# Kernel tuning notes

Measured on AMD Instinct MI355X. Metric: run time of the kernel, lower is better.

The kernel has to match this reference:

```python
import jax, jax.numpy as jnp
import numpy as np

VOCAB, D_MODEL, HEADS, PAD_ID = 32000, 512, 8, 0
D_K = D_MODEL // HEADS
EPS = 1e-5


def pos_encoding(T, d):
    pos = jnp.arange(T, dtype=jnp.float32)[:, None]              # [T,1]
    freqs = 1.0 / (10000.0 ** (jnp.arange(0, d, 2, dtype=jnp.float32) / d))
    ang = pos * freqs                                            # [T,d/2]
    pe = jnp.zeros((T, d), dtype=jnp.float32)
    pe = pe.at[:, 0::2].set(jnp.sin(ang)).at[:, 1::2].set(jnp.cos(ang))
    return pe


def layer_norm(x, g, b):
    mu = jnp.mean(x, axis=-1, keepdims=True)
    var = jnp.var(x, axis=-1, keepdims=True)
    return (x - mu) * jax.lax.rsqrt(var + EPS) * g + b


def setup_inputs() -> dict:
    key = jax.random.key(0)
    ks = jax.random.split(key, 12)
    B, T = 4, 2048
    s = 0.02
    inp = {
        "tokens": jax.random.randint(ks[0], (B, T), 0, VOCAB),
        "emb": jax.random.normal(ks[1], (VOCAB, D_MODEL), jnp.float32) * s,
        "wq": jax.random.normal(ks[2], (D_MODEL, D_MODEL), jnp.float32) * s,
        "bq": jnp.zeros((D_MODEL,), jnp.float32),
        "wk": jax.random.normal(ks[3], (D_MODEL, D_MODEL), jnp.float32) * s,
        "bk": jnp.zeros((D_MODEL,), jnp.float32),
        "wv": jax.random.normal(ks[4], (D_MODEL, D_MODEL), jnp.float32) * s,
        "bv": jnp.zeros((D_MODEL,), jnp.float32),
        "wo": jax.random.normal(ks[5], (D_MODEL, D_MODEL), jnp.float32) * s,
        "bo": jnp.zeros((D_MODEL,), jnp.float32),
        "w1": jax.random.normal(ks[6], (D_MODEL, 2 * D_MODEL), jnp.float32) * s,
        "b1": jnp.zeros((2 * D_MODEL,), jnp.float32),
        "w2": jax.random.normal(ks[7], (2 * D_MODEL, D_MODEL), jnp.float32) * s,
        "b2": jnp.zeros((D_MODEL,), jnp.float32),
        "ln1_g": jnp.ones((D_MODEL,), jnp.float32),
        "ln1_b": jnp.zeros((D_MODEL,), jnp.float32),
        "ln2_g": jnp.ones((D_MODEL,), jnp.float32),
        "ln2_b": jnp.zeros((D_MODEL,), jnp.float32),
    }
    return inp


def reference(tokens, emb, wq, bq, wk, bk, wv, bv, wo, bo,
              w1, b1, w2, b2, ln1_g, ln1_b, ln2_g, ln2_b):
    B, T = tokens.shape
    x = emb[tokens] * jnp.sqrt(jnp.float32(D_MODEL))             # [B,T,D]
    x = x + pos_encoding(T, D_MODEL)[None]                       # add PE
    q = (x @ wq + bq).reshape(B, T, HEADS, D_K)
    k = (x @ wk + bk).reshape(B, T, HEADS, D_K)
    v = (x @ wv + bv).reshape(B, T, HEADS, D_K)
    scores = jnp.einsum("bqhd,bkhd->bhqk", q, k) / jnp.sqrt(jnp.float32(D_K))
    key_pad_mask = tokens == PAD_ID                              # [B,T]
    neg = jnp.finfo(scores.dtype).min
    scores = jnp.where(key_pad_mask[:, None, None, :], neg, scores)
    attn = jax.nn.softmax(scores, axis=-1)                       # [B,H,T,T]
    av = jnp.einsum("bhqk,bkhd->bqhd", attn, v).reshape(B, T, D_MODEL)
    av = av @ wo + bo
    h = layer_norm(av + x, ln1_g, ln1_b)
    ff = jax.nn.relu(h @ w1 + b1) @ w2 + b2
    out = layer_norm(h + ff, ln2_g, ln2_b)
    return out, key_pad_mask
```

## Files before the change

kernel.cpp:

```cpp
#include <hip/hip_runtime.h>
#include <hip/hip_bf16.h>
#include <math.h>

#define D_MODEL 512
#define HEADS   8
#define D_K     64
#define T_SEQ   2048
#define B_SZ    4
#define NROWS   (B_SZ * T_SEQ)
#define KVB     64
#define KSPLIT  2
#define KHALF   (T_SEQ / KSPLIT)

#define BKG 64

typedef __attribute__((ext_vector_type(8))) short short8;
typedef __attribute__((ext_vector_type(4))) float f32x4;
typedef __attribute__((ext_vector_type(4))) ushort bf16x4;
typedef __attribute__((ext_vector_type(4))) unsigned int u32x4;

typedef __attribute__((address_space(1))) const unsigned int as1_uint;
typedef __attribute__((address_space(3))) unsigned int as3_uint;

__device__ __forceinline__ ushort f2bf(float f) {
    union { float f; unsigned u; } v; v.f = f;
    unsigned u = v.u;
    unsigned r = (u + 0x7FFFu + ((u >> 16) & 1u)) >> 16;
    return (ushort)r;
}
__device__ __forceinline__ float bf2f(ushort u) {
    union { unsigned u; float f; } v; v.u = ((unsigned)u) << 16;
    return v.f;
}
__device__ __forceinline__ unsigned pk_bf16(float lo, float hi) {
    unsigned r;
    asm("v_cvt_pk_bf16_f32 %0, %1, %2" : "=v"(r) : "v"(lo), "v"(hi));
    return r;
}

__global__ __launch_bounds__(256) void k_prep(
    const int* __restrict__ tokens, const float* __restrict__ emb,
    const float* __restrict__ wq, const float* __restrict__ wk,
    const float* __restrict__ wv, const float* __restrict__ wo,
    const float* __restrict__ w1, const float* __restrict__ w2,
    const float* __restrict__ bq, const float* __restrict__ bk,
    const float* __restrict__ bv,
    ushort* __restrict__ xb, float* __restrict__ mask_out,
    ushort* __restrict__ wqkvT, ushort* __restrict__ woT,
    ushort* __restrict__ w1T, ushort* __restrict__ w2T,
    float* __restrict__ bqkv, float qsc)
{
    __shared__ ushort tls[32][33];
    int bid = blockIdx.x, tid = threadIdx.x;
    if (bid < 4096) {
        int row = bid * 2 + (tid >> 7);
        int t   = row & (T_SEQ - 1);
        int tok = tokens[row];
        int t2  = tid & 127;
        if (t2 == 0) mask_out[row] = (tok == 0) ? 1.0f : 0.0f;
        const float* e = emb + (size_t)tok * D_MODEL;
#pragma unroll
        for (int i = 0; i < 4; ++i) {
            int d = t2 + 128 * i;
            float freq = exp2f(-(float)(d & ~1) * 0.025952563240330564f);
            float sn, cs;
            __sincosf((float)t * freq, &sn, &cs);
            float x = e[d] * 22.627416997969522f + ((d & 1) ? cs : sn);
            xb[(size_t)row * D_MODEL + d] = f2bf(x);
        }
        return;
    }
    const float* src; ushort* dst; float scale = 1.0f; int K, N, bx, by;
    if (bid < 5120) {
        int b = bid - 4096; int z = b >> 8; int rem = b & 255;
        bx = rem & 15; by = rem >> 4; K = 512; N = 512;
        src = (z == 0) ? wq : (z == 1) ? wk : (z == 2) ? wv : wo;
        dst = (z < 3) ? wqkvT + (size_t)z * 512 * 512 : woT;
        scale = (z == 0) ? qsc : 1.0f;
    } else if (bid < 5632) {
        int b = bid - 5120; bx = b & 31; by = b >> 5; K = 512; N = 1024; src = w1; dst = w1T;
    } else if (bid < 6144) {
        int b = bid - 5632; bx = b & 15; by = b >> 4; K = 1024; N = 512; src = w2; dst = w2T;
    } else {
        int i = (bid - 6144) * 256 + tid;
        if (i < 512)       bqkv[i] = bq[i] * qsc;
        else if (i < 1024) bqkv[i] = bk[i - 512];
        else if (i < 1536) bqkv[i] = bv[i - 1024];
        return;
    }
    int tx = tid & 31, ty = tid >> 5;
    int n0 = bx * 32, k0 = by * 32;
#pragma unroll
    for (int i = 0; i < 4; ++i)
        tls[ty + i * 8][tx] = f2bf(src[(size_t)(k0 + ty + i * 8) * N + n0 + tx] * scale);
    __syncthreads();
#pragma unroll
    for (int i = 0; i < 4; ++i)
        dst[(size_t)(n0 + ty + i * 8) * K + k0 + tx] = tls[tx][ty + i * 8];
}

template<int MODE, bool RELU, int BMT, int BNT, bool COMBA>
__global__ __launch_bounds__(256) void k_gemm_lds(
    const ushort* __restrict__ A, const ushort* __restrict__ A2,
    const float* __restrict__ lpb,
    const ushort* __restrict__ BT,
    const float* __restrict__ bias, void* __restrict__ C0,
    void* __restrict__ C1, void* __restrict__ C2,
    int M, int N, int K)
{
    constexpr int MR = BMT / 32;
    constexpr int NR = BNT / 32;
    __shared__ __attribute__((aligned(16))) ushort As[2][BMT * BKG];
    __shared__ __attribute__((aligned(16))) ushort Bs[2][BNT * BKG];

    const int tid = threadIdx.x;
    const int w = tid >> 6, l = tid & 63;
    const int lr = l & 15, lg = l >> 4;
    const int wr = w >> 1, wc = w & 1;

    int bx = blockIdx.x, by = blockIdx.y;
    {
        int nx = gridDim.x, ny = gridDim.y;
        if ((ny & 7) == 0) {
            int lin = bx + nx * by;
            int xcd = lin & 7, idx = lin >> 3;
            int per = ny >> 3;
            by = xcd * per + (idx % per);
            bx = idx / per;
        }
    }
    const int brow0 = by * BMT;
    const int bcol0 = bx * BNT;
    const int swz = lr & 7;

    f32x4 acc[MR][NR] = {};
    const int nks = K >> 6;

#define STAGE_B(buf, k0)                                                        \
    {                                                                           \
        _Pragma("unroll")                                                       \
        for (int i = 0; i < BNT / 32; ++i) {                                    \
            int gi = w * (BNT * 2) + i * 64 + l;                                \
            int row = gi >> 3, slot = gi & 7;                                   \
            int g = slot ^ (row & 7);                                           \
            __builtin_amdgcn_global_load_lds(                                   \
                (as1_uint*)(BT + (size_t)(bcol0 + row) * K + (k0) + g * 8),     \
                (as3_uint*)(&Bs[buf][gi * 8]), 16, 0, 0);                       \
        }                                                                       \
    }
#define STAGE_A_DMA(buf, k0)                                                    \
    {                                                                           \
        _Pragma("unroll")                                                       \
        for (int i = 0; i < BMT / 32; ++i) {                                    \
            int gi = w * (BMT * 2) + i * 64 + l;                                \
            int row = gi >> 3, slot = gi & 7;                                   \
            int g = slot ^ (row & 7);                                           \
            __builtin_amdgcn_global_load_lds(                                   \
                (as1_uint*)(A + (size_t)(brow0 + row) * K + (k0) + g * 8),      \
                (as3_uint*)(&As[buf][gi * 8]), 16, 0, 0);                       \
        }                                                                       \
    }
#define STAGE_A_COMB(buf, k0)                                                   \
    {                                                                           \
        int head = (k0) >> 6;                                                   \
        _Pragma("unroll")                                                       \
        for (int i = 0; i < BMT / 32; ++i) {                                    \
            int gi = w * (BMT * 2) + i * 64 + l;                                \
            int row = gi >> 3, slot = gi & 7;                                   \
            int g = slot ^ (row & 7);                                           \
            size_t off = (size_t)(brow0 + row) * K + (k0) + g * 8;              \
            bf16x4 a0 = *(const bf16x4*)(A + off);                              \
            bf16x4 a1 = *(const bf16x4*)(A + off + 4);                          \
            bf16x4 c0 = *(const bf16x4*)(A2 + off);                             \
            bf16x4 c1 = *(const bf16x4*)(A2 + off + 4);                         \
            float l0 = lpb[(size_t)head * NROWS + brow0 + row];                 \
            float l1 = lpb[(size_t)(8 + head) * NROWS + brow0 + row];           \
            float r = 1.0f / (l0 + l1);                                         \
            u32x4 pk;                                                           \
            pk[0] = pk_bf16((bf2f(a0[0]) + bf2f(c0[0])) * r,                    \
                            (bf2f(a0[1]) + bf2f(c0[1])) * r);                   \
            pk[1] = pk_bf16((bf2f(a0[2]) + bf2f(c0[2])) * r,                    \
                            (bf2f(a0[3]) + bf2f(c0[3])) * r);                   \
            pk[2] = pk_bf16((bf2f(a1[0]) + bf2f(c1[0])) * r,                    \
                            (bf2f(a1[1]) + bf2f(c1[1])) * r);                   \
            pk[3] = pk_bf16((bf2f(a1[2]) + bf2f(c1[2])) * r,                    \
                            (bf2f(a1[3]) + bf2f(c1[3])) * r);                   \
            *(u32x4*)(&As[buf][gi * 8]) = pk;                                   \
        }                                                                       \
    }
#define STAGE(buf, k0)                                                          \
    {                                                                           \
        if constexpr (COMBA) { STAGE_A_COMB(buf, k0); }                         \
        else                 { STAGE_A_DMA(buf, k0); }                          \
        STAGE_B(buf, k0);                                                       \
    }

    STAGE(0, 0);
    __syncthreads();

    int buf = 0;
    for (int ks = 0; ks < nks; ++ks) {
        if (ks + 1 < nks) STAGE(buf ^ 1, (ks + 1) * BKG);
#pragma unroll
        for (int kk = 0; kk < 2; ++kk) {
            short8 af[MR], bfr[NR];
#pragma unroll
            for (int m = 0; m < MR; ++m) {
                int row = wr * (BMT / 2) + m * 16 + lr;
                int slot = (kk * 4 + lg) ^ swz;
                af[m] = *(const short8*)(&As[buf][row * 64 + slot * 8]);
            }
#pragma unroll
            for (int n = 0; n < NR; ++n) {
                int row = wc * (BNT / 2) + n * 16 + lr;
                int slot = (kk * 4 + lg) ^ swz;
                bfr[n] = *(const short8*)(&Bs[buf][row * 64 + slot * 8]);
            }
#pragma unroll
            for (int m = 0; m < MR; ++m)
#pragma unroll
                for (int n = 0; n < NR; ++n)
                    acc[m][n] = __builtin_amdgcn_mfma_f32_16x16x32_bf16(af[m], bfr[n], acc[m][n], 0, 0, 0);
        }
        __syncthreads();
        buf ^= 1;
    }
#undef STAGE
#undef STAGE_A_COMB
#undef STAGE_A_DMA
#undef STAGE_B

#pragma unroll
    for (int n = 0; n < NR; ++n) {
        int col = bcol0 + wc * (BNT / 2) + n * 16 + lr;
        float bv = bias[col];
#pragma unroll
        for (int m = 0; m < MR; ++m) {
            int row0 = brow0 + wr * (BMT / 2) + m * 16 + 4 * lg;
            if constexpr (MODE == 2) {
                int seg = col >> 9, lc = col & 511;
                if (seg == 2) {
                    bf16x4 pk;
#pragma unroll
                    for (int j = 0; j < 4; ++j) pk[j] = f2bf(acc[m][n][j] + bv);
                    *(bf16x4*)((ushort*)C2 + (size_t)lc * M + row0) = pk;
                } else {
                    ushort* dst = (seg == 0) ? (ushort*)C0 : (ushort*)C1;
#pragma unroll
                    for (int j = 0; j < 4; ++j)
                        dst[(size_t)(row0 + j) * 512 + lc] = f2bf(acc[m][n][j] + bv);
                }
            } else if constexpr (MODE == 0) {
#pragma unroll
                for (int j = 0; j < 4; ++j) {
                    float v = acc[m][n][j] + bv;
                    if (RELU) v = fmaxf(v, 0.0f);
                    ((ushort*)C0)[(size_t)(row0 + j) * N + col] = f2bf(v);
                }
            } else {
#pragma unroll
                for (int j = 0; j < 4; ++j)
                    ((float*)C0)[(size_t)(row0 + j) * N + col] = acc[m][n][j] + bv;
            }
        }
    }
}

__global__ __launch_bounds__(512, 4) void k_attn(
    const ushort* __restrict__ Q, const ushort* __restrict__ Kb,
    const ushort* __restrict__ Vt, const int* __restrict__ tokens,
    ushort* __restrict__ O0, ushort* __restrict__ O1,
    float* __restrict__ lp)
{
    __shared__ __attribute__((aligned(16))) ushort Kl[2][KVB * 64];
    __shared__ __attribute__((aligned(16))) ushort Vl[2][KVB * 64];
    __shared__ __attribute__((aligned(16))) ushort Mbh[KHALF];
    __shared__ int padf[KHALF / KVB];

    const int tid = threadIdx.x;
    const int w = tid >> 6, l = tid & 63;
    const int lr = l & 15, lg = l >> 4;
    const int swz = lr & 7;

    int lin = blockIdx.x + 8 * (blockIdx.y + 8 * blockIdx.z);
    int xcd = lin & 7, idx = lin >> 3;
    int qt  = idx & 7;
    int grp = xcd + 8 * (idx >> 3);
    int ks  = grp & 1;
    int h   = (grp >> 1) & 7;
    int b   = grp >> 4;

    const int q0  = qt * 256 + w * 32;
    const int kb0 = ks * KHALF;

    const int gi   = w * 64 + l;
    const int srow = gi >> 3;
    const int sg   = gi & 7;
    const int sgx  = sg ^ (srow & 7);
    const ushort* Ksrc = Kb + ((size_t)(b * T_SEQ + kb0) + srow) * D_MODEL + h * D_K + sgx * 8;
    const int kbase = 32 * (sg >> 2) + 8 * ((sg >> 1) & 1) + 4 * (sg & 1);
    const ushort* Vsrc = Vt + (size_t)(h * D_K + srow) * NROWS + b * T_SEQ + kb0 + kbase;
    const int vds = srow * 128 + sgx * 16;

#define KSTAGE(bufi, kt_)                                                       \
    __builtin_amdgcn_global_load_lds(                                           \
        (as1_uint*)(Ksrc + (size_t)(kt_) * KVB * D_MODEL),                      \
        (as3_uint*)(&Kl[bufi][gi * 8]), 16, 0, 0);

    const ushort* Qh = Q + (size_t)b * T_SEQ * D_MODEL + h * D_K;
    short8 aq[2][2];
#pragma unroll
    for (int qs = 0; qs < 2; ++qs)
#pragma unroll
        for (int c2 = 0; c2 < 2; ++c2)
            aq[qs][c2] = *(const short8*)(Qh + (size_t)(q0 + qs * 16 + lr) * D_MODEL
                                          + c2 * 32 + 8 * lg);

    short8 vones;
#pragma unroll
    for (int i = 0; i < 8; ++i) vones[i] = (short)0x3F80;

    const int* tk = tokens + b * T_SEQ + kb0;
#pragma unroll
    for (int it = 0; it < KHALF / 512; ++it) {
        int i = tid + it * 512;
        bool pad = (tk[i] == 0);
        Mbh[i] = pad ? (ushort)0xFF7F : (ushort)0;
        unsigned long long bal = __ballot(pad);
        if (l == 0) padf[it * 8 + w] = (bal != 0ull);
    }

    f32x4 acc[2][4] = {};
    f32x4 acc_l[2] = {};

    {
        bf16x4 va = *(const bf16x4*)(Vsrc);
        bf16x4 vb2 = *(const bf16x4*)(Vsrc + 16);
        KSTAGE(0, 0);
        u32x4 pk = { ((const unsigned*)&va)[0], ((const unsigned*)&va)[1],
                     ((const unsigned*)&vb2)[0], ((const unsigned*)&vb2)[1] };
        *(u32x4*)((char*)Vl[0] + vds) = pk;
    }
    __syncthreads();

    int buf = 0;
    const int NT = KHALF / KVB;
#pragma unroll 2
    for (int kt = 0; kt < NT; ++kt) {
        bf16x4 vna, vnb;
        bool more = (kt + 1 < NT);
        if (more) {
            KSTAGE(buf ^ 1, kt + 1);
            vna = *(const bf16x4*)(Vsrc + (kt + 1) * KVB);
            vnb = *(const bf16x4*)(Vsrc + (kt + 1) * KVB + 16);
        }

        const ushort* Kt = Kl[buf];
        const ushort* Vb = Vl[buf];
        bool havePad = padf[kt];

        unsigned dw[2][4][2];
#pragma unroll
        for (int kh = 0; kh < 2; ++kh) {
            short8 kf[2][2];
#pragma unroll
            for (int i = 0; i < 2; ++i)
#pragma unroll
                for (int c2 = 0; c2 < 2; ++c2)
                    kf[i][c2] = *(const short8*)((const char*)Kt
                                + ((2 * kh + i) * 16 + lr) * 128
                                + (((c2 * 4 + lg) ^ swz) * 16));
#pragma unroll
            for (int qs = 0; qs < 2; ++qs)
#pragma unroll
                for (int i = 0; i < 2; ++i) {
                    int kb = 2 * kh + i;
                    __builtin_amdgcn_s_setprio(1);
                    f32x4 sf = {};
                    sf = __builtin_amdgcn_mfma_f32_16x16x32_bf16(kf[i][0], aq[qs][0], sf, 0, 0, 0);
                    sf = __builtin_amdgcn_mfma_f32_16x16x32_bf16(kf[i][1], aq[qs][1], sf, 0, 0, 0);
                    __builtin_amdgcn_s_setprio(0);
                    if (havePad) {
                        bf16x4 m4 = *(const bf16x4*)(Mbh + kt * KVB + kb * 16 + 4 * lg);
#pragma unroll
                        for (int j = 0; j < 4; ++j) sf[j] += bf2f(m4[j]);
                    }
                    dw[qs][kb][0] = pk_bf16(exp2f(sf[0]), exp2f(sf[1]));
                    dw[qs][kb][1] = pk_bf16(exp2f(sf[2]), exp2f(sf[3]));
                }
        }

#pragma unroll
        for (int ch = 0; ch < 2; ++ch) {
            short8 vf[2][2];
#pragma unroll
            for (int i = 0; i < 2; ++i)
#pragma unroll
                for (int kk = 0; kk < 2; ++kk)
                    vf[i][kk] = *(const short8*)((const char*)Vb
                                + ((2 * ch + i) * 16 + lr) * 128
                                + (((kk * 4 + lg) ^ swz) * 16));
            __builtin_amdgcn_s_setprio(1);
#pragma unroll
            for (int qs = 0; qs < 2; ++qs) {
                u32x4 pw0 = { dw[qs][0][0], dw[qs][0][1], dw[qs][1][0], dw[qs][1][1] };
                u32x4 pw1 = { dw[qs][2][0], dw[qs][2][1], dw[qs][3][0], dw[qs][3][1] };
                short8 pa0 = __builtin_bit_cast(short8, pw0);
                short8 pa1 = __builtin_bit_cast(short8, pw1);
#pragma unroll
                for (int i = 0; i < 2; ++i) {
                    int c = 2 * ch + i;
                    acc[qs][c] = __builtin_amdgcn_mfma_f32_16x16x32_bf16(vf[i][0], pa0, acc[qs][c], 0, 0, 0);
                    acc[qs][c] = __builtin_amdgcn_mfma_f32_16x16x32_bf16(vf[i][1], pa1, acc[qs][c], 0, 0, 0);
                }
                if (ch == 0) {
                    acc_l[qs] = __builtin_amdgcn_mfma_f32_16x16x32_bf16(vones, pa0, acc_l[qs], 0, 0, 0);
                    acc_l[qs] = __builtin_amdgcn_mfma_f32_16x16x32_bf16(vones, pa1, acc_l[qs], 0, 0, 0);
                }
            }
            __builtin_amdgcn_s_setprio(0);
        }

        if (more) {
            u32x4 pk = { ((const unsigned*)&vna)[0], ((const unsigned*)&vna)[1],
                         ((const unsigned*)&vnb)[0], ((const unsigned*)&vnb)[1] };
            *(u32x4*)((char*)Vl[buf ^ 1] + vds) = pk;
        }
        __syncthreads();
        buf ^= 1;
    }
#undef KSTAGE

    ushort* Op = (ks == 0) ? O0 : O1;
#pragma unroll
    for (int qs = 0; qs < 2; ++qs) {
        ushort* orow = Op + (size_t)(b * T_SEQ + q0 + qs * 16 + lr) * D_MODEL + h * D_K;
#pragma unroll
        for (int c = 0; c < 4; ++c) {
            bf16x4 pk;
#pragma unroll
            for (int j = 0; j < 4; ++j) pk[j] = f2bf(acc[qs][c][j]);
            *(bf16x4*)(orow + c * 16 + 4 * lg) = pk;
        }
        if (l < 16)
            lp[(size_t)(ks * 8 + h) * NROWS + b * T_SEQ + q0 + qs * 16 + l] = acc_l[qs][0];
    }
}

template<bool A_BF16, bool RES_BF16, bool OUT_F32>
__global__ __launch_bounds__(256) void k_ln(
    const void* __restrict__ A, const void* __restrict__ Res,
    const float* __restrict__ g, const float* __restrict__ bb,
    float* __restrict__ of, ushort* __restrict__ ob)
{
    int row = blockIdx.x * 4 + (threadIdx.x >> 6);
    int l = threadIdx.x & 63;
    float v[8];
    float s = 0.0f, ss = 0.0f;
#pragma unroll
    for (int i = 0; i < 2; ++i) {
        int d0 = i * 256 + l * 4;
        f32x4 va, vb;
        if (A_BF16) {
            bf16x4 t = *(const bf16x4*)((const ushort*)A + (size_t)row * D_MODEL + d0);
#pragma unroll
            for (int j = 0; j < 4; ++j) va[j] = bf2f(t[j]);
        } else {
            va = *(const f32x4*)((const float*)A + (size_t)row * D_MODEL + d0);
        }
        if (RES_BF16) {
            bf16x4 t = *(const bf16x4*)((const ushort*)Res + (size_t)row * D_MODEL + d0);
#pragma unroll
            for (int j = 0; j < 4; ++j) vb[j] = bf2f(t[j]);
        } else {
            vb = *(const f32x4*)((const float*)Res + (size_t)row * D_MODEL + d0);
        }
#pragma unroll
        for (int j = 0; j < 4; ++j) {
            float x = va[j] + vb[j];
            v[i * 4 + j] = x; s += x; ss += x * x;
        }
    }
#pragma unroll
    for (int d = 1; d < 64; d <<= 1) { s += __shfl_xor(s, d); ss += __shfl_xor(ss, d); }
    float mu  = s * (1.0f / 512.0f);
    float var = ss * (1.0f / 512.0f) - mu * mu;
    float rs  = rsqrtf(var + 1e-5f);
#pragma unroll
    for (int i = 0; i < 2; ++i)
#pragma unroll
        for (int j = 0; j < 4; ++j) {
            int d = i * 256 + l * 4 + j;
            float o = (v[i * 4 + j] - mu) * rs * g[d] + bb[d];
            if (OUT_F32) of[(size_t)row * D_MODEL + d] = o;
            else         ob[(size_t)row * D_MODEL + d] = f2bf(o);
        }
}

extern "C" void kernel_launch(void* const* d_in, const int* in_sizes, int n_in,
                              void* d_out, int out_size, void* d_ws, size_t ws_size,
                              hipStream_t stream)
{
    const int*   tokens = (const int*)  d_in[0];
    const float* emb    = (const float*)d_in[1];
    const float* wq     = (const float*)d_in[2];
    const float* bq     = (const float*)d_in[3];
    const float* wk     = (const float*)d_in[4];
    const float* bk     = (const float*)d_in[5];
    const float* wv     = (const float*)d_in[6];
    const float* bv     = (const float*)d_in[7];
    const float* wo     = (const float*)d_in[8];
    const float* bo     = (const float*)d_in[9];
    const float* w1     = (const float*)d_in[10];
    const float* b1     = (const float*)d_in[11];
    const float* w2     = (const float*)d_in[12];
    const float* b2     = (const float*)d_in[13];
    const float* ln1_g  = (const float*)d_in[14];
    const float* ln1_b  = (const float*)d_in[15];
    const float* ln2_g  = (const float*)d_in[16];
    const float* ln2_b  = (const float*)d_in[17];

    char* ws = (char*)d_ws;
    ushort* xb   = (ushort*)(ws + 0);
    ushort* Qb   = (ushort*)(ws + 8388608);
    ushort* Kbuf = (ushort*)(ws + 16777216);
    ushort* Vt   = (ushort*)(ws + 25165824);
    ushort* atb  = (ushort*)(ws + 33554432);
    ushort* AVb  = (ushort*)(ws + 41943040);
    ushort* wqkvT = (ushort*)(ws + 50331648);
    ushort* woT  = wqkvT + 1536 * 512;
    ushort* w1T  = woT + 262144;
    ushort* w2T  = w1T + 524288;
    float*  bqkv = (float*)(w2T + 524288);
    float*  lpart = bqkv + 2048;

    ushort* ff1b = Kbuf;
    ushort* ff2b = AVb;

    float* out_f    = (float*)d_out;
    float* mask_out = out_f + (size_t)NROWS * D_MODEL;

    const float QSC = 0.18033688011112042f;

    k_prep<<<6150, 256, 0, stream>>>(
        tokens, emb, wq, wk, wv, wo, w1, w2, bq, bk, bv,
        xb, mask_out, wqkvT, woT, w1T, w2T, bqkv, QSC);

    k_gemm_lds<2, false, 64, 128, false><<<dim3(12, 128), 256, 0, stream>>>(
        xb, nullptr, nullptr, wqkvT, bqkv, Qb, Kbuf, Vt, NROWS, 1536, 512);

    k_attn<<<dim3(8, 8, 8), 512, 0, stream>>>(
        Qb, Kbuf, Vt, tokens, atb, AVb, lpart);

    k_gemm_lds<0, false, 64, 64, true><<<dim3(8, 128), 256, 0, stream>>>(
        atb, AVb, lpart, woT, bo, Qb, nullptr, nullptr, NROWS, 512, 512);

    k_ln<true, true, false><<<NROWS / 4, 256, 0, stream>>>(
        Qb, xb, ln1_g, ln1_b, nullptr, atb);

    k_gemm_lds<0, true, 64, 64, false><<<dim3(16, 128), 256, 0, stream>>>(
        atb, nullptr, nullptr, w1T, b1, ff1b, nullptr, nullptr, NROWS, 1024, 512);
    k_gemm_lds<0, false, 64, 64, false><<<dim3(8, 128), 256, 0, stream>>>(
        ff1b, nullptr, nullptr, w2T, b2, ff2b, nullptr, nullptr, NROWS, 512, 1024);

    k_ln<true, true, true><<<NROWS / 4, 256, 0, stream>>>(
        ff2b, atb, ln2_g, ln2_b, out_f, nullptr);
}
```

Measured before the change: 144.8 us.

## Pre-permute V^T in projection epilogue and stage V via direct global-to-LDS loads

The QKV projection epilogue now writes the transposed V with a permuted key order inside each 64-key block, so the layout the attention kernel needs already exists in global memory. The attention kernel can then load V tiles with the same async global_load_lds path used for K, instead of loading into registers, repacking, and storing to LDS after compute. This removes VGPR pressure and the register round-trip, and it overlaps the V transfer with compute. It relies on the permutation matching the MFMA consumer layout exactly.

```diff
diff --git a/kernel.cpp b/kernel.cpp
--- a/kernel.cpp
+++ b/kernel.cpp
@@ -243,7 +243,10 @@
                     bf16x4 pk;
 #pragma unroll
                     for (int j = 0; j < 4; ++j) pk[j] = f2bf(acc[m][n][j] + bv);
-                    *(bf16x4*)((ushort*)C2 + (size_t)lc * M + row0) = pk;
+                    int kg  = (row0 >> 2) & 15;
+                    int pos = (row0 & ~63) + ((kg & 8) << 2) + ((kg & 2) << 3)
+                              + ((kg & 1) << 3) + (kg & 4);
+                    *(bf16x4*)((ushort*)C2 + (size_t)lc * M + pos) = pk;
                 } else {
                     ushort* dst = (seg == 0) ? (ushort*)C0 : (ushort*)C1;
 #pragma unroll
@@ -298,14 +301,17 @@
     const int sg   = gi & 7;
     const int sgx  = sg ^ (srow & 7);
     const ushort* Ksrc = Kb + ((size_t)(b * T_SEQ + kb0) + srow) * D_MODEL + h * D_K + sgx * 8;
-    const int kbase = 32 * (sg >> 2) + 8 * ((sg >> 1) & 1) + 4 * (sg & 1);
-    const ushort* Vsrc = Vt + (size_t)(h * D_K + srow) * NROWS + b * T_SEQ + kb0 + kbase;
-    const int vds = srow * 128 + sgx * 16;
-
-#define KSTAGE(bufi, kt_)                                                       \
-    __builtin_amdgcn_global_load_lds(                                           \
-        (as1_uint*)(Ksrc + (size_t)(kt_) * KVB * D_MODEL),                      \
-        (as3_uint*)(&Kl[bufi][gi * 8]), 16, 0, 0);
+    const ushort* Vsrc = Vt + (size_t)(h * D_K + srow) * NROWS + b * T_SEQ + kb0 + sgx * 8;
+
+#define KVSTAGE(bufi, kt_)                                                      \
+    {                                                                           \
+        __builtin_amdgcn_global_load_lds(                                       \
+            (as1_uint*)(Ksrc + (size_t)(kt_) * KVB * D_MODEL),                  \
+            (as3_uint*)(&Kl[bufi][gi * 8]), 16, 0, 0);                          \
+        __builtin_amdgcn_global_load_lds(                                       \
+            (as1_uint*)(Vsrc + (kt_) * KVB),                                    \
+            (as3_uint*)(&Vl[bufi][gi * 8]), 16, 0, 0);                          \
+    }
 
     const ushort* Qh = Q + (size_t)b * T_SEQ * D_MODEL + h * D_K;
     short8 aq[2][2];
@@ -333,27 +339,14 @@
     f32x4 acc[2][4] = {};
     f32x4 acc_l[2] = {};
 
-    {
-        bf16x4 va = *(const bf16x4*)(Vsrc);
-        bf16x4 vb2 = *(const bf16x4*)(Vsrc + 16);
-        KSTAGE(0, 0);
-        u32x4 pk = { ((const unsigned*)&va)[0], ((const unsigned*)&va)[1],
-                     ((const unsigned*)&vb2)[0], ((const unsigned*)&vb2)[1] };
-        *(u32x4*)((char*)Vl[0] + vds) = pk;
-    }
+    KVSTAGE(0, 0);
     __syncthreads();
 
     int buf = 0;
     const int NT = KHALF / KVB;
 #pragma unroll 2
     for (int kt = 0; kt < NT; ++kt) {
-        bf16x4 vna, vnb;
-        bool more = (kt + 1 < NT);
-        if (more) {
-            KSTAGE(buf ^ 1, kt + 1);
-            vna = *(const bf16x4*)(Vsrc + (kt + 1) * KVB);
-            vnb = *(const bf16x4*)(Vsrc + (kt + 1) * KVB + 16);
-        }
+        if (kt + 1 < NT) KVSTAGE(buf ^ 1, kt + 1);
 
         const ushort* Kt = Kl[buf];
         const ushort* Vb = Vl[buf];
@@ -421,15 +414,10 @@
             __builtin_amdgcn_s_setprio(0);
         }
 
-        if (more) {
-            u32x4 pk = { ((const unsigned*)&vna)[0], ((const unsigned*)&vna)[1],
-                         ((const unsigned*)&vnb)[0], ((const unsigned*)&vnb)[1] };
-            *(u32x4*)((char*)Vl[buf ^ 1] + vds) = pk;
-        }
         __syncthreads();
         buf ^= 1;
     }
-#undef KSTAGE
+#undef KVSTAGE
 
     ushort* Op = (ks == 0) ? O0 : O1;
 #pragma unroll
```

New measurement: 144.3 us. No clear change (-0.3%).
